# Performance work log

Measured on AMD Instinct MI355X. Metric: run time of the kernel, lower is better.

## Reference

```python
import jax, jax.numpy as jnp
import numpy as np
import math

B, L, DIM = 128, 192, 512
NTOKEN = 100
MAX_BONDS = 6
MAX_LEN = 192


def _sinusoidal_pe(max_len, dim):
    pos = np.arange(max_len, dtype=np.float32)[:, None]
    div = np.exp(np.arange(0, dim, 2, dtype=np.float32) * (-math.log(10000.0) / dim))
    pe = np.zeros((max_len, dim), dtype=np.float32)
    pe[:, 0::2] = np.sin(pos * div)
    pe[:, 1::2] = np.cos(pos * div)
    return jnp.asarray(pe[:, None, :])  # [max_len, 1, dim]


def setup_inputs() -> dict:
    key = jax.random.key(0)
    ks = jax.random.split(key, 16)
    s = 0.02
    inp = {
        "element": jax.random.randint(ks[0], (B, L), 0, NTOKEN),
        "bond": jax.random.randint(ks[1], (B, L, MAX_BONDS), 0, L),
        "aroma": jax.random.randint(ks[2], (B, L), 0, 2),
        "charge": jax.random.randint(ks[3], (B, L), 0, 6),
        "segment": jax.random.randint(ks[4], (B, L), 0, 30),
        # parameters
        "pe": _sinusoidal_pe(MAX_LEN, DIM),
        "E_elem": jax.random.normal(ks[5], (NTOKEN, DIM), jnp.float32) * s,
        "E_charge": jax.random.normal(ks[6], (13, DIM), jnp.float32) * s,
        "E_aroma": jax.random.normal(ks[7], (2, DIM), jnp.float32) * s,
        "E_seg": jax.random.normal(ks[8], (30, DIM), jnp.float32) * s,
        "W1": jax.random.normal(ks[9], (DIM, 4 * DIM), jnp.float32) * s,
        "b1": jnp.zeros((4 * DIM,), jnp.float32),
        "W2": jax.random.normal(ks[10], (4 * DIM, DIM), jnp.float32) * s,
        "b2": jnp.zeros((DIM,), jnp.float32),
        "W3": jax.random.normal(ks[11], (DIM, 4 * DIM), jnp.float32) * s,
        "b3": jnp.zeros((4 * DIM,), jnp.float32),
        "W4": jax.random.normal(ks[12], (4 * DIM, DIM), jnp.float32) * s,
        "b4": jnp.zeros((DIM,), jnp.float32),
        "W5": jax.random.normal(ks[13], (DIM, DIM), jnp.float32) * s,
        "b5": jnp.zeros((DIM,), jnp.float32),
    }
    return inp


def _mlp(x, W1, b1, W2, b2, W3, b3, W4, b4, W5, b5):
    x = x + jnp.maximum(x @ W1 + b1, 0.0) @ W2 + b2
    x = x + jnp.maximum(x @ W3 + b3, 0.0) @ W4 + b4
    return x @ W5 + b5


def reference(element, bond, aroma, charge, segment, pe,
              E_elem, E_charge, E_aroma, E_seg,
              W1, b1, W2, b2, W3, b3, W4, b4, W5, b5):
    b, l = element.shape
    # embeddings: all [l, b, dim]
    emb = E_elem[element.T]
    emb = emb + pe[:l]                      # [l,1,dim] broadcast (eval: dropout off)
    emb = emb + E_aroma[aroma.T]
    emb = emb + E_charge[charge.T + 6]
    emb = emb + E_seg[segment.T]
    message = _mlp(emb, W1, b1, W2, b2, W3, b3, W4, b4, W5, b5)  # [l,b,dim]
    # bond aggregation: agg[k] = sum_m message[bond[b,k,m]] excluding self-bonds
    # (equivalent to the dense one-hot einsum with the diagonal masked out)
    msg_bld = jnp.transpose(message, (1, 0, 2))          # [b,l,dim]
    g = msg_bld[jnp.arange(b)[:, None, None], bond]      # [b,l,MAX_BONDS,dim]
    mask = (bond != jnp.arange(l)[None, :, None]).astype(message.dtype)
    agg = jnp.einsum('bkmd,bkm->bkd', g, mask)           # [b,l,dim]
    return emb + jnp.transpose(agg, (1, 0, 2))           # [l,b,dim]
```

## Files before the change

kernel.cpp:

```cpp
#include <hip/hip_runtime.h>
#include <cstdint>
#include <cstddef>

typedef unsigned short u16;
typedef unsigned int u32;

typedef unsigned short u16x8 __attribute__((ext_vector_type(8)));
typedef __bf16 bf16x8 __attribute__((ext_vector_type(8)));
typedef float f32x4 __attribute__((ext_vector_type(4)));
typedef float f32x8 __attribute__((ext_vector_type(8)));

#define NB   128
#define NL   192
#define NTOK (NB * NL)
#define DIM  512
#define HID  2048

static __device__ __forceinline__ float bf2f(u16 h) {
    union { u32 u; float f; } v; v.u = ((u32)h) << 16; return v.f;
}
static __device__ __forceinline__ u16 f2bf(float f) {
    union { float f; u32 u; } v; v.f = f;
    u32 u = v.u + 0x7FFF + ((v.u >> 16) & 1);
    return (u16)(u >> 16);
}

__global__ void transpose_f2b(const float* __restrict__ in, u16* __restrict__ out,
                              int K, int N) {
    __shared__ float tile[32][33];
    int tx = threadIdx.x & 31, ty = threadIdx.x >> 5;
    int n0 = blockIdx.x * 32, k0 = blockIdx.y * 32;
#pragma unroll
    for (int i = 0; i < 4; i++)
        tile[ty + i * 8][tx] = in[(size_t)(k0 + ty + i * 8) * N + n0 + tx];
    __syncthreads();
#pragma unroll
    for (int i = 0; i < 4; i++)
        out[(size_t)(n0 + ty + i * 8) * K + k0 + tx] = f2bf(tile[tx][ty + i * 8]);
}

static __device__ __forceinline__ void add8f(float* acc, const float* p) {
    f32x8 v = *(const f32x8*)p;
#pragma unroll
    for (int i = 0; i < 8; i++) acc[i] += v[i];
}

__global__ void embed_kernel(const int* __restrict__ element, const int* __restrict__ aroma,
                             const int* __restrict__ charge, const int* __restrict__ segment,
                             const float* __restrict__ pe, const float* __restrict__ E_elem,
                             const float* __restrict__ E_charge, const float* __restrict__ E_aroma,
                             const float* __restrict__ E_seg,
                             float* __restrict__ emb32, u16* __restrict__ emb16) {
    int t = blockIdx.x * 4 + (threadIdx.x >> 6);
    int lane = threadIdx.x & 63;
    int l = t >> 7, b = t & 127;
    int d = lane * 8;
    int idx = b * NL + l;
    int e = element[idx];
    int a = aroma[idx];
    int c = charge[idx] + 6;
    int s = segment[idx];
    float acc[8] = {0, 0, 0, 0, 0, 0, 0, 0};
    add8f(acc, E_elem  + (size_t)e * DIM + d);
    add8f(acc, pe      + (size_t)l * DIM + d);
    add8f(acc, E_aroma + (size_t)a * DIM + d);
    add8f(acc, E_charge+ (size_t)c * DIM + d);
    add8f(acc, E_seg   + (size_t)s * DIM + d);
    f32x8 o32; u16x8 o16;
#pragma unroll
    for (int i = 0; i < 8; i++) { o32[i] = acc[i]; o16[i] = f2bf(acc[i]); }
    *(f32x8*)(emb32 + (size_t)t * DIM + d) = o32;
    *(u16x8*)(emb16 + (size_t)t * DIM + d) = o16;
}

__global__ __launch_bounds__(512, 2) void gemm_bt(
    const u16* __restrict__ A, const u16* __restrict__ BT,
    const float* __restrict__ bias, const u16* __restrict__ resid16,
    const float* __restrict__ resid32,
    u16* __restrict__ C, int M, int N, int K, int do_relu) {
    __shared__ __align__(16) u16 smem[256 * 264];

    const int tid  = threadIdx.x;
    const int wave = tid >> 6;
    const int lane = tid & 63;

    const int nwg = gridDim.x;
    const int bid = blockIdx.x;
    const int wg  = ((nwg & 7) == 0) ? ((bid & 7) * (nwg >> 3) + (bid >> 3)) : bid;
    const int nt  = N >> 8;
    const int m0  = (wg / nt) * 256;
    const int n0  = (wg % nt) * 256;

    const int wmh = wave >> 2;
    const int wnq = wave & 3;
    const int fr  = lane & 15;
    const int fq  = lane >> 4;
    const int ck0 = ((fq ^ (fr & 7)) * 8);
    const int ck1 = (((4 | fq) ^ (fr & 7)) * 8);

    const int sRow = tid >> 3;
    const int sChk = ((tid & 7) ^ (sRow & 7)) * 8;
    const int ldst = sRow * 64 + (tid & 7) * 8;

    const u16* Asrc = A  + (size_t)(m0 + sRow) * K + sChk;
    const u16* Bsrc = BT + (size_t)(n0 + sRow) * K + sChk;

    f32x4 acc[8][4] = {};

#define GLL(gp, lp) __builtin_amdgcn_global_load_lds(                            \
        (const __attribute__((address_space(1))) void*)(gp),                     \
        (__attribute__((address_space(3))) void*)(lp), 16, 0, 0)
#define STAGE(buf, kt) do {                                                      \
    GLL(Asrc + (size_t)(kt) * 64,                 &smem[(buf)*16384 +        ldst]); \
    GLL(Bsrc + (size_t)(kt) * 64,                 &smem[32768 + (buf)*16384 +        ldst]); \
    GLL(Asrc + (size_t)(kt) * 64 + (size_t) 64*K, &smem[(buf)*16384 +  4096 + ldst]); \
    GLL(Bsrc + (size_t)(kt) * 64 + (size_t) 64*K, &smem[32768 + (buf)*16384 +  4096 + ldst]); \
    GLL(Asrc + (size_t)(kt) * 64 + (size_t)128*K, &smem[(buf)*16384 +  8192 + ldst]); \
    GLL(Bsrc + (size_t)(kt) * 64 + (size_t)128*K, &smem[32768 + (buf)*16384 +  8192 + ldst]); \
    GLL(Asrc + (size_t)(kt) * 64 + (size_t)192*K, &smem[(buf)*16384 + 12288 + ldst]); \
    GLL(Bsrc + (size_t)(kt) * 64 + (size_t)192*K, &smem[32768 + (buf)*16384 + 12288 + ldst]); \
} while (0)

    const int nk = K >> 6;
    STAGE(0, 0);

    for (int t = 0; t < nk; ++t) {
        asm volatile("s_waitcnt vmcnt(0)\n\ts_barrier" ::: "memory");
        if (t + 1 < nk) STAGE((t + 1) & 1, t + 1);

        const u16* Ab = &smem[(t & 1) * 16384];
        const u16* Bb = &smem[32768 + (t & 1) * 16384];
#pragma unroll
        for (int s = 0; s < 2; ++s) {
            const int ck = s ? ck1 : ck0;
            bf16x8 af[8], bg[4];
#pragma unroll
            for (int i = 0; i < 8; ++i)
                af[i] = *(const bf16x8*)(&Ab[(wmh * 128 + i * 16 + fr) * 64 + ck]);
#pragma unroll
            for (int j = 0; j < 4; ++j)
                bg[j] = *(const bf16x8*)(&Bb[(wnq * 64 + j * 16 + fr) * 64 + ck]);

            __builtin_amdgcn_s_setprio(1);
#pragma unroll
            for (int i = 0; i < 8; ++i)
#pragma unroll
                for (int j = 0; j < 4; ++j)
                    acc[i][j] = __builtin_amdgcn_mfma_f32_16x16x32_bf16(
                        af[i], bg[j], acc[i][j], 0, 0, 0);
            __builtin_amdgcn_s_setprio(0);
        }
    }
#undef STAGE
#undef GLL

    __syncthreads();
#define CSTR 264
#pragma unroll
    for (int j = 0; j < 4; j++) {
        int n = n0 + wnq * 64 + j * 16 + fr;
        float bv = bias[n];
#pragma unroll
        for (int i = 0; i < 8; i++) {
#pragma unroll
            for (int r = 0; r < 4; r++) {
                int m = m0 + wmh * 128 + i * 16 + fq * 4 + r;
                float v = acc[i][j][r] + bv;
                if (do_relu) v = fmaxf(v, 0.0f);
                if (resid16) v += bf2f(resid16[(size_t)m * N + n]);
                if (resid32) v += resid32[(size_t)m * N + n];
                smem[(wmh * 128 + i * 16 + fq * 4 + r) * CSTR + wnq * 64 + j * 16 + fr] = f2bf(v);
            }
        }
    }
    __syncthreads();
    {
        const int erow = tid >> 5;
        const int ecol = (tid & 31) * 8;
#pragma unroll
        for (int rr = 0; rr < 16; ++rr) {
            int row = rr * 16 + erow;
            *(u16x8*)(C + (size_t)(m0 + row) * N + n0 + ecol) =
                *(const u16x8*)(&smem[row * CSTR + ecol]);
        }
    }
#undef CSTR
}

__global__ void agg_kernel(const float* __restrict__ emb32, const u16* __restrict__ msg,
                           const int* __restrict__ bond, float* __restrict__ out) {
    int t = blockIdx.x * 4 + (threadIdx.x >> 6);
    int lane = threadIdx.x & 63;
    int l = t >> 7, b = t & 127;
    int d = lane * 8;
    float acc[8];
    {
        f32x8 v = *(const f32x8*)(emb32 + (size_t)t * DIM + d);
#pragma unroll
        for (int i = 0; i < 8; i++) acc[i] = v[i];
    }
    const int* bp = bond + ((size_t)b * NL + l) * 6;
#pragma unroll
    for (int m = 0; m < 6; m++) {
        int j = bp[m];
        if (j != l) {
            u16x8 g = *(const u16x8*)(msg + ((size_t)j * NB + b) * DIM + d);
#pragma unroll
            for (int i = 0; i < 8; i++) acc[i] += bf2f(g[i]);
        }
    }
    f32x8 o;
#pragma unroll
    for (int i = 0; i < 8; i++) o[i] = acc[i];
    *(f32x8*)(out + (size_t)t * DIM + d) = o;
}

extern "C" void kernel_launch(void* const* d_in, const int* in_sizes, int n_in,
                              void* d_out, int out_size, void* d_ws, size_t ws_size,
                              hipStream_t stream) {
    const int* element = (const int*)d_in[0];
    const int* bond    = (const int*)d_in[1];
    const int* aroma   = (const int*)d_in[2];
    const int* charge  = (const int*)d_in[3];
    const int* segment = (const int*)d_in[4];
    const float* pe      = (const float*)d_in[5];
    const float* E_elem  = (const float*)d_in[6];
    const float* E_charge= (const float*)d_in[7];
    const float* E_aroma = (const float*)d_in[8];
    const float* E_seg   = (const float*)d_in[9];
    const float* W1 = (const float*)d_in[10];
    const float* b1 = (const float*)d_in[11];
    const float* W2 = (const float*)d_in[12];
    const float* b2 = (const float*)d_in[13];
    const float* W3 = (const float*)d_in[14];
    const float* b3 = (const float*)d_in[15];
    const float* W4 = (const float*)d_in[16];
    const float* b4 = (const float*)d_in[17];
    const float* W5 = (const float*)d_in[18];
    const float* b5 = (const float*)d_in[19];

    float* emb32 = (float*)d_out;

    char* ws = (char*)d_ws;
    size_t woff = 0;
    auto take = [&](size_t bytes) -> u16* {
        u16* p = (u16*)(ws + woff);
        woff += (bytes + 255) & ~(size_t)255;
        return p;
    };
    u16* W1T = take((size_t)HID * DIM * 2);
    u16* W2T = take((size_t)DIM * HID * 2);
    u16* W3T = take((size_t)HID * DIM * 2);
    u16* W4T = take((size_t)DIM * HID * 2);
    u16* W5T = take((size_t)DIM * DIM * 2);
    u16* emb16 = take((size_t)NTOK * DIM * 2);
    u16* msg   = take((size_t)NTOK * DIM * 2);

    static const int ncs[] = {1, 2, 3, 4, 6, 8, 12, 16, 24, 32, 48, 96};
    int CM = 256;
    for (int nc : ncs) {
        int cm = NTOK / nc;
        if (cm % 256 != 0) continue;
        size_t need = woff + ((size_t)cm * HID * 2 + 256)
                           + ((size_t)cm * DIM * 2 + 256) * 2;
        if (need <= ws_size) { CM = cm; break; }
    }
    u16* hC  = take((size_t)CM * HID * 2);
    u16* xaC = take((size_t)CM * DIM * 2);
    u16* xbC = take((size_t)CM * DIM * 2);

    transpose_f2b<<<dim3(HID / 32, DIM / 32), 256, 0, stream>>>(W1, W1T, DIM, HID);
    transpose_f2b<<<dim3(DIM / 32, HID / 32), 256, 0, stream>>>(W2, W2T, HID, DIM);
    transpose_f2b<<<dim3(HID / 32, DIM / 32), 256, 0, stream>>>(W3, W3T, DIM, HID);
    transpose_f2b<<<dim3(DIM / 32, HID / 32), 256, 0, stream>>>(W4, W4T, HID, DIM);
    transpose_f2b<<<dim3(DIM / 32, DIM / 32), 256, 0, stream>>>(W5, W5T, DIM, DIM);

    embed_kernel<<<NTOK / 4, 256, 0, stream>>>(element, aroma, charge, segment, pe,
                                               E_elem, E_charge, E_aroma, E_seg,
                                               emb32, emb16);

    for (int c0 = 0; c0 < NTOK; c0 += CM) {
        const u16* x16 = emb16 + (size_t)c0 * DIM;
        const float* x32 = emb32 + (size_t)c0 * DIM;
        u16* msgC = msg + (size_t)c0 * DIM;
        int mt = CM / 256;
        gemm_bt<<<dim3(mt * (HID / 256)), 512, 0, stream>>>(x16, W1T, b1, nullptr, nullptr, hC,  CM, HID, DIM, 1);
        gemm_bt<<<dim3(mt * (DIM / 256)), 512, 0, stream>>>(hC,  W2T, b2, nullptr, x32,     xaC, CM, DIM, HID, 0);
        gemm_bt<<<dim3(mt * (HID / 256)), 512, 0, stream>>>(xaC, W3T, b3, nullptr, nullptr, hC,  CM, HID, DIM, 1);
        gemm_bt<<<dim3(mt * (DIM / 256)), 512, 0, stream>>>(hC,  W4T, b4, xaC,    nullptr,  xbC, CM, DIM, HID, 0);
        gemm_bt<<<dim3(mt * (DIM / 256)), 512, 0, stream>>>(xbC, W5T, b5, nullptr, nullptr, msgC, CM, DIM, DIM, 0);
    }

    agg_kernel<<<NTOK / 4, 256, 0, stream>>>(emb32, msg, bond, (float*)d_out);
}
```

Measured before the change: 487.7 us.

## Fuse FFN blocks into per-row-tile kernels keeping hidden activations on-chip

Replaces the five separate tiled GEMM launches (with a chunked global hidden buffer) with two fused FFN kernels. Each block owns 96 token rows, keeps its input tile and a 256-wide slice of the hidden activation in shared memory, and accumulates the down-projection in registers. The second kernel also applies the residual and the final W5 projection in place. This removes the global round-trip of the 2048-wide hidden tensor and several launches. In exchange, weight fragments are read directly from global memory without LDS staging, there are many block-wide barriers per hidden slice, and register pressure is high.

```diff
diff --git a/kernel.cpp b/kernel.cpp
--- a/kernel.cpp
+++ b/kernel.cpp
@@ -15,6 +15,7 @@
 #define NTOK (NB * NL)
 #define DIM  512
 #define HID  2048
+#define PM   96
 
 static __device__ __forceinline__ float bf2f(u16 h) {
     union { u32 u; float f; } v; v.u = ((u32)h) << 16; return v.f;
@@ -73,118 +74,231 @@
     *(u16x8*)(emb16 + (size_t)t * DIM + d) = o16;
 }
 
-__global__ __launch_bounds__(512, 2) void gemm_bt(
-    const u16* __restrict__ A, const u16* __restrict__ BT,
-    const float* __restrict__ bias, const u16* __restrict__ resid16,
+__global__ __launch_bounds__(512, 2) void ffn_fused(
+    const u16* __restrict__ X,
     const float* __restrict__ resid32,
-    u16* __restrict__ C, int M, int N, int K, int do_relu) {
-    __shared__ __align__(16) u16 smem[256 * 264];
+    const u16* __restrict__ WaT,
+    const float* __restrict__ ba,
+    const u16* __restrict__ WbT,
+    const float* __restrict__ bb,
+    const u16* __restrict__ WcT,
+    const float* __restrict__ bc,
+    u16* __restrict__ OUT) {
+    __shared__ __align__(16) u16 xs[PM * 512];
+    __shared__ __align__(16) u16 hs[PM * 264];
 
     const int tid  = threadIdx.x;
     const int wave = tid >> 6;
     const int lane = tid & 63;
-
-    const int nwg = gridDim.x;
+    const int fr   = lane & 15;
+    const int fq   = lane >> 4;
+    const int wmh  = wave >> 2;
+    const int wnq  = wave & 3;
+
     const int bid = blockIdx.x;
-    const int wg  = ((nwg & 7) == 0) ? ((bid & 7) * (nwg >> 3) + (bid >> 3)) : bid;
-    const int nt  = N >> 8;
-    const int m0  = (wg / nt) * 256;
-    const int n0  = (wg % nt) * 256;
-
-    const int wmh = wave >> 2;
-    const int wnq = wave & 3;
-    const int fr  = lane & 15;
-    const int fq  = lane >> 4;
-    const int ck0 = ((fq ^ (fr & 7)) * 8);
-    const int ck1 = (((4 | fq) ^ (fr & 7)) * 8);
-
-    const int sRow = tid >> 3;
-    const int sChk = ((tid & 7) ^ (sRow & 7)) * 8;
-    const int ldst = sRow * 64 + (tid & 7) * 8;
-
-    const u16* Asrc = A  + (size_t)(m0 + sRow) * K + sChk;
-    const u16* Bsrc = BT + (size_t)(n0 + sRow) * K + sChk;
-
-    f32x4 acc[8][4] = {};
+    const int wg  = (bid & 7) * (gridDim.x >> 3) + (bid >> 3);
+    const int m0  = wg * PM;
 
 #define GLL(gp, lp) __builtin_amdgcn_global_load_lds(                            \
         (const __attribute__((address_space(1))) void*)(gp),                     \
         (__attribute__((address_space(3))) void*)(lp), 16, 0, 0)
-#define STAGE(buf, kt) do {                                                      \
-    GLL(Asrc + (size_t)(kt) * 64,                 &smem[(buf)*16384 +        ldst]); \
-    GLL(Bsrc + (size_t)(kt) * 64,                 &smem[32768 + (buf)*16384 +        ldst]); \
-    GLL(Asrc + (size_t)(kt) * 64 + (size_t) 64*K, &smem[(buf)*16384 +  4096 + ldst]); \
-    GLL(Bsrc + (size_t)(kt) * 64 + (size_t) 64*K, &smem[32768 + (buf)*16384 +  4096 + ldst]); \
-    GLL(Asrc + (size_t)(kt) * 64 + (size_t)128*K, &smem[(buf)*16384 +  8192 + ldst]); \
-    GLL(Bsrc + (size_t)(kt) * 64 + (size_t)128*K, &smem[32768 + (buf)*16384 +  8192 + ldst]); \
-    GLL(Asrc + (size_t)(kt) * 64 + (size_t)192*K, &smem[(buf)*16384 + 12288 + ldst]); \
-    GLL(Bsrc + (size_t)(kt) * 64 + (size_t)192*K, &smem[32768 + (buf)*16384 + 12288 + ldst]); \
-} while (0)
-
-    const int nk = K >> 6;
-    STAGE(0, 0);
-
-    for (int t = 0; t < nk; ++t) {
-        asm volatile("s_waitcnt vmcnt(0)\n\ts_barrier" ::: "memory");
-        if (t + 1 < nk) STAGE((t + 1) & 1, t + 1);
-
-        const u16* Ab = &smem[(t & 1) * 16384];
-        const u16* Bb = &smem[32768 + (t & 1) * 16384];
-#pragma unroll
-        for (int s = 0; s < 2; ++s) {
-            const int ck = s ? ck1 : ck0;
-            bf16x8 af[8], bg[4];
-#pragma unroll
-            for (int i = 0; i < 8; ++i)
-                af[i] = *(const bf16x8*)(&Ab[(wmh * 128 + i * 16 + fr) * 64 + ck]);
-#pragma unroll
-            for (int j = 0; j < 4; ++j)
-                bg[j] = *(const bf16x8*)(&Bb[(wnq * 64 + j * 16 + fr) * 64 + ck]);
-
+#pragma unroll
+    for (int g = 0; g < 12; ++g) {
+        int chunk = g * 512 + tid;
+        int row = chunk >> 6, c = chunk & 63;
+        GLL(X + (size_t)(m0 + row) * 512 + ((c ^ (row & 7)) * 8), &xs[chunk * 8]);
+    }
+#undef GLL
+    asm volatile("s_waitcnt vmcnt(0)" ::: "memory");
+    __syncthreads();
+
+#define XRD(row, q) (*(const bf16x8*)&xs[(row) * 512 + (((q) ^ ((row) & 7)) * 8)])
+
+    f32x4 acc2[3][8] = {};
+
+    for (int j = 0; j < 8; ++j) {
+        f32x4 acc1[3][4] = {};
+        const u16* Wa = WaT + (size_t)(j * 256 + wnq * 64) * 512;
+#pragma unroll
+        for (int kt = 0; kt < 8; ++kt) {
+            bf16x8 bfr[4][2], afr[3][2];
+#pragma unroll
+            for (int j2 = 0; j2 < 4; ++j2)
+#pragma unroll
+                for (int s = 0; s < 2; ++s)
+                    bfr[j2][s] = *(const bf16x8*)(Wa + (size_t)(j2 * 16 + fr) * 512
+                                                  + kt * 64 + s * 32 + fq * 8);
+#pragma unroll
+            for (int i = 0; i < 3; ++i) {
+                int row = wmh * 48 + i * 16 + fr;
+#pragma unroll
+                for (int s = 0; s < 2; ++s)
+                    afr[i][s] = XRD(row, kt * 8 + s * 4 + fq);
+            }
             __builtin_amdgcn_s_setprio(1);
 #pragma unroll
-            for (int i = 0; i < 8; ++i)
-#pragma unroll
-                for (int j = 0; j < 4; ++j)
-                    acc[i][j] = __builtin_amdgcn_mfma_f32_16x16x32_bf16(
-                        af[i], bg[j], acc[i][j], 0, 0, 0);
+            for (int i = 0; i < 3; ++i)
+#pragma unroll
+                for (int j2 = 0; j2 < 4; ++j2)
+#pragma unroll
+                    for (int s = 0; s < 2; ++s)
+                        acc1[i][j2] = __builtin_amdgcn_mfma_f32_16x16x32_bf16(
+                            afr[i][s], bfr[j2][s], acc1[i][j2], 0, 0, 0);
             __builtin_amdgcn_s_setprio(0);
         }
-    }
-#undef STAGE
-#undef GLL
+        __syncthreads();
+#pragma unroll
+        for (int j2 = 0; j2 < 4; ++j2) {
+            float bv = ba[j * 256 + wnq * 64 + j2 * 16 + fr];
+#pragma unroll
+            for (int i = 0; i < 3; ++i)
+#pragma unroll
+                for (int r = 0; r < 4; ++r)
+                    hs[(wmh * 48 + i * 16 + fq * 4 + r) * 264 + wnq * 64 + j2 * 16 + fr]
+                        = f2bf(fmaxf(acc1[i][j2][r] + bv, 0.0f));
+        }
+        __syncthreads();
+        const u16* Wb = WbT + (size_t)(wnq * 128) * 2048 + j * 256;
+#pragma unroll
+        for (int k2t = 0; k2t < 4; ++k2t) {
+            bf16x8 afr[3][2];
+#pragma unroll
+            for (int i = 0; i < 3; ++i)
+#pragma unroll
+                for (int s = 0; s < 2; ++s)
+                    afr[i][s] = *(const bf16x8*)&hs[(wmh * 48 + i * 16 + fr) * 264
+                                                    + k2t * 64 + s * 32 + fq * 8];
+#pragma unroll
+            for (int hb = 0; hb < 2; ++hb) {
+                bf16x8 bfr[4][2];
+#pragma unroll
+                for (int j2 = 0; j2 < 4; ++j2)
+#pragma unroll
+                    for (int s = 0; s < 2; ++s)
+                        bfr[j2][s] = *(const bf16x8*)(Wb + (size_t)((hb * 4 + j2) * 16 + fr) * 2048
+                                                      + k2t * 64 + s * 32 + fq * 8);
+                __builtin_amdgcn_s_setprio(1);
+#pragma unroll
+                for (int i = 0; i < 3; ++i)
+#pragma unroll
+                    for (int j2 = 0; j2 < 4; ++j2)
+#pragma unroll
+                        for (int s = 0; s < 2; ++s)
+                            acc2[i][hb * 4 + j2] = __builtin_amdgcn_mfma_f32_16x16x32_bf16(
+                                afr[i][s], bfr[j2][s], acc2[i][hb * 4 + j2], 0, 0, 0);
+                __builtin_amdgcn_s_setprio(0);
+            }
+        }
+    }
+
+    if (!WcT) {
+#pragma unroll
+        for (int p = 0; p < 2; ++p) {
+            __syncthreads();
+            if ((wnq >> 1) == p) {
+#pragma unroll
+                for (int j2 = 0; j2 < 8; ++j2) {
+                    int col = wnq * 128 + j2 * 16 + fr;
+                    float bv = bb[col];
+#pragma unroll
+                    for (int i = 0; i < 3; ++i)
+#pragma unroll
+                        for (int r = 0; r < 4; ++r) {
+                            int row = wmh * 48 + i * 16 + fq * 4 + r;
+                            float v = acc2[i][j2][r] + bv
+                                    + resid32[(size_t)(m0 + row) * 512 + col];
+                            hs[row * 264 + (col - p * 256)] = f2bf(v);
+                        }
+                }
+            }
+            __syncthreads();
+#pragma unroll
+            for (int g = 0; g < 6; ++g) {
+                int chunk = g * 512 + tid;
+                int row = chunk >> 5, c = chunk & 31;
+                *(u16x8*)(OUT + (size_t)(m0 + row) * 512 + p * 256 + c * 8) =
+                    *(const u16x8*)&hs[row * 264 + c * 8];
+            }
+        }
+        return;
+    }
 
     __syncthreads();
-#define CSTR 264
-#pragma unroll
-    for (int j = 0; j < 4; j++) {
-        int n = n0 + wnq * 64 + j * 16 + fr;
-        float bv = bias[n];
-#pragma unroll
-        for (int i = 0; i < 8; i++) {
-#pragma unroll
-            for (int r = 0; r < 4; r++) {
-                int m = m0 + wmh * 128 + i * 16 + fq * 4 + r;
-                float v = acc[i][j][r] + bv;
-                if (do_relu) v = fmaxf(v, 0.0f);
-                if (resid16) v += bf2f(resid16[(size_t)m * N + n]);
-                if (resid32) v += resid32[(size_t)m * N + n];
-                smem[(wmh * 128 + i * 16 + fq * 4 + r) * CSTR + wnq * 64 + j * 16 + fr] = f2bf(v);
-            }
-        }
+#pragma unroll
+    for (int j2 = 0; j2 < 8; ++j2) {
+        int col = wnq * 128 + j2 * 16 + fr;
+        float bv = bb[col];
+        int q = col >> 3, lo = col & 7;
+#pragma unroll
+        for (int i = 0; i < 3; ++i)
+#pragma unroll
+            for (int r = 0; r < 4; ++r) {
+                int row = wmh * 48 + i * 16 + fq * 4 + r;
+                int xi = row * 512 + ((q ^ (row & 7)) * 8) + lo;
+                float v = acc2[i][j2][r] + bv + bf2f(xs[xi]);
+                xs[xi] = f2bf(v);
+            }
     }
     __syncthreads();
-    {
-        const int erow = tid >> 5;
-        const int ecol = (tid & 31) * 8;
-#pragma unroll
-        for (int rr = 0; rr < 16; ++rr) {
-            int row = rr * 16 + erow;
-            *(u16x8*)(C + (size_t)(m0 + row) * N + n0 + ecol) =
-                *(const u16x8*)(&smem[row * CSTR + ecol]);
-        }
-    }
-#undef CSTR
+    f32x4 acc3[3][8] = {};
+#pragma unroll
+    for (int kt = 0; kt < 8; ++kt) {
+        bf16x8 afr[3][2];
+#pragma unroll
+        for (int i = 0; i < 3; ++i) {
+            int row = wmh * 48 + i * 16 + fr;
+#pragma unroll
+            for (int s = 0; s < 2; ++s)
+                afr[i][s] = XRD(row, kt * 8 + s * 4 + fq);
+        }
+#pragma unroll
+        for (int hb = 0; hb < 2; ++hb) {
+            bf16x8 bfr[4][2];
+#pragma unroll
+            for (int j2 = 0; j2 < 4; ++j2)
+#pragma unroll
+                for (int s = 0; s < 2; ++s)
+                    bfr[j2][s] = *(const bf16x8*)(WcT + (size_t)(wnq * 128 + (hb * 4 + j2) * 16 + fr) * 512
+                                                  + kt * 64 + s * 32 + fq * 8);
+            __builtin_amdgcn_s_setprio(1);
+#pragma unroll
+            for (int i = 0; i < 3; ++i)
+#pragma unroll
+                for (int j2 = 0; j2 < 4; ++j2)
+#pragma unroll
+                    for (int s = 0; s < 2; ++s)
+                        acc3[i][hb * 4 + j2] = __builtin_amdgcn_mfma_f32_16x16x32_bf16(
+                            afr[i][s], bfr[j2][s], acc3[i][hb * 4 + j2], 0, 0, 0);
+            __builtin_amdgcn_s_setprio(0);
+        }
+    }
+#pragma unroll
+    for (int p = 0; p < 2; ++p) {
+        __syncthreads();
+        if ((wnq >> 1) == p) {
+#pragma unroll
+            for (int j2 = 0; j2 < 8; ++j2) {
+                int col = wnq * 128 + j2 * 16 + fr;
+                float bv = bc[col];
+#pragma unroll
+                for (int i = 0; i < 3; ++i)
+#pragma unroll
+                    for (int r = 0; r < 4; ++r) {
+                        int row = wmh * 48 + i * 16 + fq * 4 + r;
+                        hs[row * 264 + (col - p * 256)] = f2bf(acc3[i][j2][r] + bv);
+                    }
+            }
+        }
+        __syncthreads();
+#pragma unroll
+        for (int g = 0; g < 6; ++g) {
+            int chunk = g * 512 + tid;
+            int row = chunk >> 5, c = chunk & 31;
+            *(u16x8*)(OUT + (size_t)(m0 + row) * 512 + p * 256 + c * 8) =
+                *(const u16x8*)&hs[row * 264 + c * 8];
+        }
+    }
+#undef XRD
 }
 
 __global__ void agg_kernel(const float* __restrict__ emb32, const u16* __restrict__ msg,
@@ -254,20 +368,8 @@
     u16* W4T = take((size_t)DIM * HID * 2);
     u16* W5T = take((size_t)DIM * DIM * 2);
     u16* emb16 = take((size_t)NTOK * DIM * 2);
+    u16* xa    = take((size_t)NTOK * DIM * 2);
     u16* msg   = take((size_t)NTOK * DIM * 2);
-
-    static const int ncs[] = {1, 2, 3, 4, 6, 8, 12, 16, 24, 32, 48, 96};
-    int CM = 256;
-    for (int nc : ncs) {
-        int cm = NTOK / nc;
-        if (cm % 256 != 0) continue;
-        size_t need = woff + ((size_t)cm * HID * 2 + 256)
-                           + ((size_t)cm * DIM * 2 + 256) * 2;
-        if (need <= ws_size) { CM = cm; break; }
-    }
-    u16* hC  = take((size_t)CM * HID * 2);
-    u16* xaC = take((size_t)CM * DIM * 2);
-    u16* xbC = take((size_t)CM * DIM * 2);
 
     transpose_f2b<<<dim3(HID / 32, DIM / 32), 256, 0, stream>>>(W1, W1T, DIM, HID);
     transpose_f2b<<<dim3(DIM / 32, HID / 32), 256, 0, stream>>>(W2, W2T, HID, DIM);
@@ -279,17 +381,10 @@
                                                E_elem, E_charge, E_aroma, E_seg,
                                                emb32, emb16);
 
-    for (int c0 = 0; c0 < NTOK; c0 += CM) {
-        const u16* x16 = emb16 + (size_t)c0 * DIM;
-        const float* x32 = emb32 + (size_t)c0 * DIM;
-        u16* msgC = msg + (size_t)c0 * DIM;
-        int mt = CM / 256;
-        gemm_bt<<<dim3(mt * (HID / 256)), 512, 0, stream>>>(x16, W1T, b1, nullptr, nullptr, hC,  CM, HID, DIM, 1);
-        gemm_bt<<<dim3(mt * (DIM / 256)), 512, 0, stream>>>(hC,  W2T, b2, nullptr, x32,     xaC, CM, DIM, HID, 0);
-        gemm_bt<<<dim3(mt * (HID / 256)), 512, 0, stream>>>(xaC, W3T, b3, nullptr, nullptr, hC,  CM, HID, DIM, 1);
-        gemm_bt<<<dim3(mt * (DIM / 256)), 512, 0, stream>>>(hC,  W4T, b4, xaC,    nullptr,  xbC, CM, DIM, HID, 0);
-        gemm_bt<<<dim3(mt * (DIM / 256)), 512, 0, stream>>>(xbC, W5T, b5, nullptr, nullptr, msgC, CM, DIM, DIM, 0);
-    }
+    ffn_fused<<<NTOK / PM, 512, 0, stream>>>(emb16, emb32, W1T, b1, W2T, b2,
+                                             nullptr, nullptr, xa);
+    ffn_fused<<<NTOK / PM, 512, 0, stream>>>(xa, nullptr, W3T, b3, W4T, b4,
+                                             W5T, b5, msg);
 
     agg_kernel<<<NTOK / 4, 256, 0, stream>>>(emb32, msg, bond, (float*)d_out);
 }
```

Result: slower. 704.8 us (+44.5%).
